# Kernel optimization log

Hardware: AMD Instinct MI355X
Metric: run time of the kernel (lower is better)

## Reference

```python
import jax, jax.numpy as jnp
import numpy as np

HEAD_DIM = 32  # fixed by the module's reshape(b, d/32, 32)


def setup_inputs() -> dict:
    key = jax.random.key(0)
    kx, kw = jax.random.split(key)
    b, d = 32, 65536  # seq_len = d // 32 = 2048
    x = jax.random.normal(kx, (b, d), dtype=jnp.float32)
    # kernel: nn.init.uniform_(-0.05, 0.05), shape (3, output_dim, output_dim)
    kernel = jax.random.uniform(kw, (3, HEAD_DIM, HEAD_DIM), dtype=jnp.float32,
                                minval=-0.05, maxval=0.05)
    return {"x": x, "kernel": kernel}


def reference(x, kernel):
    b, d = x.shape
    s = d // HEAD_DIM
    xr = x.reshape(b, s, HEAD_DIM)                      # [b, s, 32]
    q = jnp.einsum('bsd,de->bse', xr, kernel[0])
    k = jnp.einsum('bsd,de->bse', xr, kernel[1])
    v = jnp.einsum('bsd,de->bse', xr, kernel[2])
    scores = jnp.einsum('bsd,btd->bst', q, k) / jnp.sqrt(jnp.float32(HEAD_DIM))
    attn = jax.nn.softmax(scores, axis=-1)              # [b, s, s]
    out = jnp.einsum('bst,btd->bsd', attn, v)           # [b, s, 32]
    return out.reshape(b, d)
```

## Files before the change

kernel.cpp:

```cpp
#include <hip/hip_runtime.h>
#include <hip/hip_bf16.h>


typedef __attribute__((ext_vector_type(8))) short bf16x8;
typedef __attribute__((ext_vector_type(4))) short bf16x4;
typedef __attribute__((ext_vector_type(4))) float f32x4;
typedef __attribute__((ext_vector_type(2))) unsigned int u32x2;
typedef __attribute__((ext_vector_type(4))) unsigned int u32x4;

#if __has_builtin(__builtin_amdgcn_mfma_f32_16x16x16bf16_1k)
#define MFMA_PV(a, b, c) __builtin_amdgcn_mfma_f32_16x16x16bf16_1k(a, b, c, 0, 0, 0)
#elif defined(__HIP_DEVICE_COMPILE__)
#error "no 16x16x16 bf16 mfma builtin on device"
#else
#define MFMA_PV(a, b, c) (c)
#endif

__device__ __forceinline__ unsigned cvt_pk_bf16(float lo, float hi) {
  unsigned r;
  asm("v_cvt_pk_bf16_f32 %0, %1, %2" : "=v"(r) : "v"(lo), "v"(hi));
  return r;
}
__device__ __forceinline__ bf16x4 as_bf16x4(u32x2 u) {
  union { u32x2 a; bf16x4 b; } c; c.a = u; return c.b;
}

__global__ __launch_bounds__(256) void qkv_kernel(
    const float* __restrict__ x, const float* __restrict__ w,
    unsigned short* __restrict__ Qb, unsigned short* __restrict__ KF,
    unsigned short* __restrict__ VP) {
  __shared__ float Wlds[1024];
  __shared__ float xs[4608];
  __shared__ __align__(16) unsigned char RP[8192];
  int tid = threadIdx.x;
  int h = blockIdx.x >> 9;
  int rb = blockIdx.x & 511;

  const float* xg = x + (size_t)(rb * 128) * 32;
#pragma unroll
  for (int k2 = 0; k2 < 4; ++k2) {
    int fi = k2 * 1024 + tid * 4;
    f32x4 v = *(const f32x4*)(xg + fi);
    *(f32x4*)(&xs[(fi >> 5) * 36 + (fi & 31)]) = v;
  }
#pragma unroll
  for (int i = 0; i < 4; ++i) Wlds[i * 256 + tid] = w[h * 1024 + i * 256 + tid];
  __syncthreads();

  int half = tid >> 7;
  int row = rb * 128 + (tid & 127);
  const float* xr = &xs[(tid & 127) * 36];
  f32x4 xv[8];
#pragma unroll
  for (int j = 0; j < 8; ++j) xv[j] = *(const f32x4*)(xr + j * 4);

  f32x4 acc[4];
#pragma unroll
  for (int j = 0; j < 4; ++j) acc[j] = (f32x4)0.0f;
#pragma unroll
  for (int d = 0; d < 32; ++d) {
    float xd = xv[d >> 2][d & 3];
    const f32x4* wr = (const f32x4*)&Wlds[d * 32 + half * 16];
#pragma unroll
    for (int j = 0; j < 4; ++j) acc[j] += xd * wr[j];
  }

  const float alpha = 1.4426950408889634f * 0.17677669529663687f;
  int L = tid & 127;

  if (h == 0) {
    u32x4 o4[2];
#pragma unroll
    for (int q = 0; q < 2; ++q)
#pragma unroll
      for (int c = 0; c < 4; ++c) {
        int e = q * 8 + c * 2;
        o4[q][c] = cvt_pk_bf16(acc[e >> 2][e & 3] * alpha, acc[(e + 1) >> 2][(e + 1) & 3] * alpha);
      }
    u32x4* dst = (u32x4*)(Qb + (size_t)row * 32 + half * 16);
    dst[0] = o4[0];
    dst[1] = o4[1];
  } else if (h == 1) {
    int kcl = L >> 6, kt = (L >> 4) & 3, n = L & 15;
    u32x4 o4[2];
#pragma unroll
    for (int q = 0; q < 2; ++q)
#pragma unroll
      for (int c = 0; c < 4; ++c) {
        int e = q * 8 + c * 2;
        o4[q][c] = cvt_pk_bf16(acc[e >> 2][e & 3], acc[(e + 1) >> 2][(e + 1) & 3]);
      }
    *(u32x4*)(RP + kcl * 4096 + kt * 1024 + (2 * half + 0) * 256 + n * 16) = o4[0];
    *(u32x4*)(RP + kcl * 4096 + kt * 1024 + (2 * half + 1) * 256 + n * 16) = o4[1];
    __syncthreads();
    char* dst = (char*)KF + (size_t)rb * 8192;
#pragma unroll
    for (int m = 0; m < 4; ++m)
      *(u32x2*)(dst + tid * 8 + m * 2048) = *(const u32x2*)(RP + tid * 8 + m * 2048);
  } else {
    unsigned short* VFlds = (unsigned short*)RP;
    int kcl = L >> 6, kt = (L >> 4) & 3, g = (L >> 2) & 3, i = L & 3;
    int base = kcl * 2048 + half * 1024 + (kt >> 1) * 512 + g * 128 + (kt & 1) * 4 + i;
#pragma unroll
    for (int nn = 0; nn < 16; ++nn) {
      unsigned r = cvt_pk_bf16(acc[nn >> 2][nn & 3], acc[nn >> 2][nn & 3]);
      VFlds[base + nn * 8] = (unsigned short)(r & 0xffffu);
    }
    __syncthreads();
    char* dst = (char*)VP + (size_t)rb * 8192;
#pragma unroll
    for (int m = 0; m < 4; ++m)
      *(u32x2*)(dst + tid * 8 + m * 2048) = *(const u32x2*)(RP + tid * 8 + m * 2048);
  }
}

#define SMAX(SF, I2) {                                           \
    float p0 = __builtin_amdgcn_exp2f(SF[0]);                    \
    float p1 = __builtin_amdgcn_exp2f(SF[1]);                    \
    float p2 = __builtin_amdgcn_exp2f(SF[2]);                    \
    float p3 = __builtin_amdgcn_exp2f(SF[3]);                    \
    lsum += (p0 + p1) + (p2 + p3);                               \
    pk[I2] = cvt_pk_bf16(p0, p1);                                \
    pk[I2 + 1] = cvt_pk_bf16(p2, p3); }

#define PVKT(KT, V0, V1, ACC0, ACC1) {                           \
    u32x2 bw; bw[0] = pk[2 * KT]; bw[1] = pk[2 * KT + 1];        \
    bf16x4 bb = as_bf16x4(bw);                                   \
    ACC0 = MFMA_PV(as_bf16x4(V0), bb, ACC0);                     \
    ACC1 = MFMA_PV(as_bf16x4(V1), bb, ACC1); }

__global__ __launch_bounds__(256, 4) void attn_kernel(
    const unsigned short* __restrict__ Qb, const unsigned short* __restrict__ KF,
    const unsigned short* __restrict__ VP, float* __restrict__ out) {
  __shared__ __align__(16) unsigned char lds[2][8192];
  unsigned char* ldsb = &lds[0][0];
  int tid = threadIdx.x;
  int wv = tid >> 6, lane = tid & 63;
  int n = lane & 15, g = lane >> 4;

  int bid = blockIdx.x;
  int swz = (bid & 7) * 128 + (bid >> 3);
  int bi = swz >> 5, qt = swz & 31;

  size_t Rq = (size_t)bi * 2048 + qt * 64 + wv * 16;

  const unsigned char* Kg = (const unsigned char*)KF + (size_t)bi * 131072;
  const unsigned char* Vg = (const unsigned char*)VP + (size_t)bi * 131072;

  const unsigned char* sgp = (wv < 2 ? Kg : Vg) + (wv & 1) * 2048 + lane * 16;
  unsigned char* ldsw = ldsb + (wv < 2 ? 0 : 4096) + (wv & 1) * 2048 + lane * 16;

  bf16x8 qf = *(const bf16x8*)(Qb + (Rq + n) * 32 + g * 8);

  f32x4 oA0 = (f32x4)0.0f, oA1 = (f32x4)0.0f;
  f32x4 oB0 = (f32x4)0.0f, oB1 = (f32x4)0.0f;
  float lsum = 0.0f;

  bf16x8 kr0, kr1;

  kr0 = *(const bf16x8*)(sgp);
  kr1 = *(const bf16x8*)(sgp + 1024);
  sgp += 4096;
  *(bf16x8*)(ldsw) = kr0;
  *(bf16x8*)(ldsw + 1024) = kr1;
  __syncthreads();

  for (int t = 0; t < 32; ++t) {
    int buf = t & 1;
    if (t < 31) {
      kr0 = *(const bf16x8*)(sgp);
      kr1 = *(const bf16x8*)(sgp + 1024);
      sgp += 4096;
    }
    const unsigned char* Lp = ldsb + buf * 8192;
    bf16x8 kf0 = *(const bf16x8*)(Lp + lane * 16);
    bf16x8 kf1 = *(const bf16x8*)(Lp + lane * 16 + 1024);
    bf16x8 kf2 = *(const bf16x8*)(Lp + lane * 16 + 2048);
    bf16x8 kf3 = *(const bf16x8*)(Lp + lane * 16 + 3072);
    u32x4 w00 = *(const u32x4*)(Lp + 4096 + lane * 16);
    u32x4 w01 = *(const u32x4*)(Lp + 4096 + lane * 16 + 1024);
    u32x4 w10 = *(const u32x4*)(Lp + 4096 + lane * 16 + 2048);
    u32x4 w11 = *(const u32x4*)(Lp + 4096 + lane * 16 + 3072);
    u32x2 vf0; vf0[0] = w00[0]; vf0[1] = w00[1];
    u32x2 vf1; vf1[0] = w00[2]; vf1[1] = w00[3];
    u32x2 vf2; vf2[0] = w01[0]; vf2[1] = w01[1];
    u32x2 vf3; vf3[0] = w01[2]; vf3[1] = w01[3];
    u32x2 vf4; vf4[0] = w10[0]; vf4[1] = w10[1];
    u32x2 vf5; vf5[0] = w10[2]; vf5[1] = w10[3];
    u32x2 vf6; vf6[0] = w11[0]; vf6[1] = w11[1];
    u32x2 vf7; vf7[0] = w11[2]; vf7[1] = w11[3];
    f32x4 s0 = __builtin_amdgcn_mfma_f32_16x16x32_bf16(kf0, qf, (f32x4)0.0f, 0, 0, 0);
    f32x4 s1 = __builtin_amdgcn_mfma_f32_16x16x32_bf16(kf1, qf, (f32x4)0.0f, 0, 0, 0);
    f32x4 s2 = __builtin_amdgcn_mfma_f32_16x16x32_bf16(kf2, qf, (f32x4)0.0f, 0, 0, 0);
    f32x4 s3 = __builtin_amdgcn_mfma_f32_16x16x32_bf16(kf3, qf, (f32x4)0.0f, 0, 0, 0);
    unsigned pk[8];
    SMAX(s0, 0) SMAX(s1, 2) SMAX(s2, 4) SMAX(s3, 6)
    PVKT(0, vf0, vf4, oA0, oA1) PVKT(1, vf1, vf5, oA0, oA1)
    PVKT(2, vf2, vf6, oB0, oB1) PVKT(3, vf3, vf7, oB0, oB1)
    __syncthreads();
    if (t < 31) {
      unsigned char* Wp = ldsw + (buf ^ 1) * 8192;
      *(bf16x8*)(Wp) = kr0;
      *(bf16x8*)(Wp + 1024) = kr1;
      __syncthreads();
    }
  }

  lsum += __shfl_xor(lsum, 16);
  lsum += __shfl_xor(lsum, 32);
  float inv = 1.0f / lsum;

  f32x4 r0 = (oA0 + oB0) * inv;
  f32x4 r1 = (oA1 + oB1) * inv;
  float* ob = out + (Rq + n) * 32 + g * 4;
  *(f32x4*)(ob)      = r0;
  *(f32x4*)(ob + 16) = r1;
}

extern "C" void kernel_launch(void* const* d_in, const int* in_sizes, int n_in,
                              void* d_out, int out_size, void* d_ws, size_t ws_size,
                              hipStream_t stream) {
  const float* x = (const float*)d_in[0];
  const float* w = (const float*)d_in[1];
  float* out = (float*)d_out;

  unsigned short* KF = (unsigned short*)d_ws;
  unsigned short* VP = KF + (size_t)65536 * 32;
  unsigned short* Qb = VP + (size_t)65536 * 32;

  qkv_kernel<<<1536, 256, 0, stream>>>(x, w, Qb, KF, VP);
  attn_kernel<<<1024, 256, 0, stream>>>(Qb, KF, VP, out);
}
```

Baseline: 48.05 us.

## Compute Q, K and V in one block per 64-row tile

The QKV projection kernel now has each block load a 64-row x tile once and compute all three projections, with 4 threads per row each producing 8 output columns, where before a separate block per head reloaded x. This cuts the x reads to a third and reduces the grid from 1536 to 1024 blocks. The cost is more registers and LDS per block, because the full weight tensor is staged, plus extra barriers to reuse the staging buffer for the K and V layouts. Only the small pre-pass changes; the attention kernel, which likely dominates, is untouched.

```diff
diff --git a/kernel.cpp b/kernel.cpp
--- a/kernel.cpp
+++ b/kernel.cpp
@@ -29,89 +29,82 @@
     const float* __restrict__ x, const float* __restrict__ w,
     unsigned short* __restrict__ Qb, unsigned short* __restrict__ KF,
     unsigned short* __restrict__ VP) {
-  __shared__ float Wlds[1024];
-  __shared__ float xs[4608];
-  __shared__ __align__(16) unsigned char RP[8192];
+  __shared__ float Wlds[3072];
+  __shared__ float xs[2304];
+  __shared__ __align__(16) unsigned char RP[4096];
   int tid = threadIdx.x;
-  int h = blockIdx.x >> 9;
-  int rb = blockIdx.x & 511;
-
-  const float* xg = x + (size_t)(rb * 128) * 32;
-#pragma unroll
-  for (int k2 = 0; k2 < 4; ++k2) {
+  int B = blockIdx.x;
+
+  const float* xg = x + (size_t)B * 2048;
+#pragma unroll
+  for (int k2 = 0; k2 < 2; ++k2) {
     int fi = k2 * 1024 + tid * 4;
     f32x4 v = *(const f32x4*)(xg + fi);
     *(f32x4*)(&xs[(fi >> 5) * 36 + (fi & 31)]) = v;
   }
 #pragma unroll
-  for (int i = 0; i < 4; ++i) Wlds[i * 256 + tid] = w[h * 1024 + i * 256 + tid];
-  __syncthreads();
-
-  int half = tid >> 7;
-  int row = rb * 128 + (tid & 127);
-  const float* xr = &xs[(tid & 127) * 36];
+  for (int i = 0; i < 12; ++i) Wlds[i * 256 + tid] = w[i * 256 + tid];
+  __syncthreads();
+
+  int L64 = tid >> 2, q = tid & 3;
+  int kt = L64 >> 4, n = L64 & 15;
+  int g4 = (L64 >> 2) & 3, i4 = L64 & 3;
+
+  const float* xr = &xs[L64 * 36];
   f32x4 xv[8];
 #pragma unroll
   for (int j = 0; j < 8; ++j) xv[j] = *(const f32x4*)(xr + j * 4);
 
-  f32x4 acc[4];
-#pragma unroll
-  for (int j = 0; j < 4; ++j) acc[j] = (f32x4)0.0f;
+  f32x4 aq0 = (f32x4)0.0f, aq1 = (f32x4)0.0f;
+  f32x4 ak0 = (f32x4)0.0f, ak1 = (f32x4)0.0f;
+  f32x4 av0 = (f32x4)0.0f, av1 = (f32x4)0.0f;
 #pragma unroll
   for (int d = 0; d < 32; ++d) {
     float xd = xv[d >> 2][d & 3];
-    const f32x4* wr = (const f32x4*)&Wlds[d * 32 + half * 16];
-#pragma unroll
-    for (int j = 0; j < 4; ++j) acc[j] += xd * wr[j];
+    const f32x4* w0 = (const f32x4*)&Wlds[d * 32 + q * 8];
+    const f32x4* w1 = (const f32x4*)&Wlds[1024 + d * 32 + q * 8];
+    const f32x4* w2 = (const f32x4*)&Wlds[2048 + d * 32 + q * 8];
+    aq0 += xd * w0[0]; aq1 += xd * w0[1];
+    ak0 += xd * w1[0]; ak1 += xd * w1[1];
+    av0 += xd * w2[0]; av1 += xd * w2[1];
   }
 
   const float alpha = 1.4426950408889634f * 0.17677669529663687f;
-  int L = tid & 127;
-
-  if (h == 0) {
-    u32x4 o4[2];
-#pragma unroll
-    for (int q = 0; q < 2; ++q)
-#pragma unroll
-      for (int c = 0; c < 4; ++c) {
-        int e = q * 8 + c * 2;
-        o4[q][c] = cvt_pk_bf16(acc[e >> 2][e & 3] * alpha, acc[(e + 1) >> 2][(e + 1) & 3] * alpha);
-      }
-    u32x4* dst = (u32x4*)(Qb + (size_t)row * 32 + half * 16);
-    dst[0] = o4[0];
-    dst[1] = o4[1];
-  } else if (h == 1) {
-    int kcl = L >> 6, kt = (L >> 4) & 3, n = L & 15;
-    u32x4 o4[2];
-#pragma unroll
-    for (int q = 0; q < 2; ++q)
-#pragma unroll
-      for (int c = 0; c < 4; ++c) {
-        int e = q * 8 + c * 2;
-        o4[q][c] = cvt_pk_bf16(acc[e >> 2][e & 3], acc[(e + 1) >> 2][(e + 1) & 3]);
-      }
-    *(u32x4*)(RP + kcl * 4096 + kt * 1024 + (2 * half + 0) * 256 + n * 16) = o4[0];
-    *(u32x4*)(RP + kcl * 4096 + kt * 1024 + (2 * half + 1) * 256 + n * 16) = o4[1];
-    __syncthreads();
-    char* dst = (char*)KF + (size_t)rb * 8192;
-#pragma unroll
-    for (int m = 0; m < 4; ++m)
-      *(u32x2*)(dst + tid * 8 + m * 2048) = *(const u32x2*)(RP + tid * 8 + m * 2048);
-  } else {
-    unsigned short* VFlds = (unsigned short*)RP;
-    int kcl = L >> 6, kt = (L >> 4) & 3, g = (L >> 2) & 3, i = L & 3;
-    int base = kcl * 2048 + half * 1024 + (kt >> 1) * 512 + g * 128 + (kt & 1) * 4 + i;
-#pragma unroll
-    for (int nn = 0; nn < 16; ++nn) {
-      unsigned r = cvt_pk_bf16(acc[nn >> 2][nn & 3], acc[nn >> 2][nn & 3]);
-      VFlds[base + nn * 8] = (unsigned short)(r & 0xffffu);
+
+  {
+    u32x4 oq;
+    oq[0] = cvt_pk_bf16(aq0[0] * alpha, aq0[1] * alpha);
+    oq[1] = cvt_pk_bf16(aq0[2] * alpha, aq0[3] * alpha);
+    oq[2] = cvt_pk_bf16(aq1[0] * alpha, aq1[1] * alpha);
+    oq[3] = cvt_pk_bf16(aq1[2] * alpha, aq1[3] * alpha);
+    *(u32x4*)(Qb + (size_t)(B * 64 + L64) * 32 + q * 8) = oq;
+  }
+
+  {
+    u32x4 ok;
+    ok[0] = cvt_pk_bf16(ak0[0], ak0[1]);
+    ok[1] = cvt_pk_bf16(ak0[2], ak0[3]);
+    ok[2] = cvt_pk_bf16(ak1[0], ak1[1]);
+    ok[3] = cvt_pk_bf16(ak1[2], ak1[3]);
+    *(u32x4*)(RP + kt * 1024 + q * 256 + n * 16) = ok;
+  }
+  __syncthreads();
+  *(u32x4*)((char*)KF + (size_t)B * 4096 + tid * 16) = *(const u32x4*)(RP + tid * 16);
+  __syncthreads();
+
+  {
+    unsigned short* Vl = (unsigned short*)RP;
+    int sbase = (q >> 1) * 1024 + (kt >> 1) * 512 + g4 * 128 + (kt & 1) * 4 + i4;
+#pragma unroll
+    for (int oo = 0; oo < 8; ++oo) {
+      float vv = (oo < 4) ? av0[oo] : av1[oo - 4];
+      unsigned r = cvt_pk_bf16(vv, vv);
+      int e = q * 8 + oo;
+      Vl[sbase + (e & 15) * 8] = (unsigned short)(r & 0xffffu);
     }
-    __syncthreads();
-    char* dst = (char*)VP + (size_t)rb * 8192;
-#pragma unroll
-    for (int m = 0; m < 4; ++m)
-      *(u32x2*)(dst + tid * 8 + m * 2048) = *(const u32x2*)(RP + tid * 8 + m * 2048);
-  }
+  }
+  __syncthreads();
+  *(u32x4*)((char*)VP + (size_t)B * 4096 + tid * 16) = *(const u32x4*)(RP + tid * 16);
 }
 
 #define SMAX(SF, I2) {                                           \
@@ -228,6 +221,6 @@
   unsigned short* VP = KF + (size_t)65536 * 32;
   unsigned short* Qb = VP + (size_t)65536 * 32;
 
-  qkv_kernel<<<1536, 256, 0, stream>>>(x, w, Qb, KF, VP);
+  qkv_kernel<<<1024, 256, 0, stream>>>(x, w, Qb, KF, VP);
   attn_kernel<<<1024, 256, 0, stream>>>(Qb, KF, VP, out);
 }
```

Result: no change. 48.97 us (+1.9%).
